# Optimization experiments

Measured on AMD Instinct MI355X. Metric: run time of the kernel, lower is better.

## Reference

```python
import jax, jax.numpy as jnp
import numpy as np

HEADS = 8
DIM_HEAD = 64

def setup_inputs() -> dict:
    key = jax.random.key(0)
    k1, k2, k3 = jax.random.split(key, 3)
    B, L, D = 8, 4096, 512
    hidden = HEADS * DIM_HEAD  # 512
    x = jax.random.normal(k1, (B, L, D), dtype=jnp.float32)
    # Conv1d(kernel_size=1) weights, squeezed to 2D matrices
    Wqkv = jax.random.normal(k2, (3 * hidden, D), dtype=jnp.float32) * (1.0 / np.sqrt(D))
    Wout = jax.random.normal(k3, (D, hidden), dtype=jnp.float32) * (1.0 / np.sqrt(hidden))
    bout = jnp.zeros((D,), dtype=jnp.float32)
    return {"x": x, "Wqkv": Wqkv, "Wout": Wout, "bout": bout}

def reference(x, Wqkv, Wout, bout):
    B, L, D = x.shape
    H, C = HEADS, DIM_HEAD
    # pointwise conv == linear over channel dim: (b, 3*H*C, l)
    qkv = jnp.einsum('bld,od->bol', x, Wqkv)
    qkv = qkv.reshape(B, 3, H, C, L)  # channel split order: (qkv, heads, c)
    q, k, v = qkv[:, 0], qkv[:, 1], qkv[:, 2]  # each (b, h, c, l)
    k = jax.nn.softmax(k, axis=-1)   # softmax over sequence
    q = jax.nn.softmax(q, axis=-2)   # softmax over feature dim (q_norm=True)
    context = jnp.einsum('bhdn,bhen->bhde', k, v)   # (b,h,c,c)
    out = jnp.einsum('bhde,bhdn->bhen', context, q)  # (b,h,c,l)
    out = out.reshape(B, H * C, L)
    y = jnp.einsum('bcl,dc->bld', out, Wout) + bout  # to_out + permute back
    return y
```

## Files before the change

### kernel.cpp

```cpp
#include <hip/hip_runtime.h>

#define L 4096
#define D 512
#define NCH 16

typedef __bf16 bf16x8 __attribute__((ext_vector_type(8)));
typedef float  f32x4  __attribute__((ext_vector_type(4)));

__device__ __forceinline__ void load_lds16(const void* g, void* l) {
    __builtin_amdgcn_global_load_lds(
        (const __attribute__((address_space(1))) void*)g,
        (__attribute__((address_space(3))) void*)l, 16, 0, 0);
}

__global__ __launch_bounds__(256) void f32_to_bf16(const float* __restrict__ in,
                                                   __bf16* __restrict__ out, int n8) {
    int i = blockIdx.x * 256 + threadIdx.x;
    if (i >= n8) return;
    const float4* p = (const float4*)in + (size_t)i * 2;
    float4 a = p[0], b = p[1];
    bf16x8 o = {(__bf16)a.x, (__bf16)a.y, (__bf16)a.z, (__bf16)a.w,
                (__bf16)b.x, (__bf16)b.y, (__bf16)b.z, (__bf16)b.w};
    *(bf16x8*)(out + (size_t)i * 8) = o;
}

template <int M, int N, int K, typename CT>
__global__ __launch_bounds__(256) void gemm_bf16_mfma(
    const __bf16* __restrict__ A, size_t aStride,
    const __bf16* __restrict__ B, size_t bStride,
    CT* __restrict__ C, size_t cStride,
    const float* __restrict__ bias) {
    __shared__ __align__(16) __bf16 sA[128 * 32];
    __shared__ __align__(16) __bf16 sB[128 * 32];
    const int b  = blockIdx.z;
    const int m0 = blockIdx.y * 128;
    const int n0 = blockIdx.x * 128;
    const int t    = threadIdx.x;
    const int wave = t >> 6, lane = t & 63;
    const int wm = (wave & 1) * 64, wn = (wave >> 1) * 64;
    const __bf16* Ab = A + (size_t)b * aStride;
    const __bf16* Bb = B + (size_t)b * bStride;
    CT* Cb = C + (size_t)b * cStride;

    f32x4 acc[4][4];
#pragma unroll
    for (int i = 0; i < 4; i++)
#pragma unroll
        for (int j = 0; j < 4; j++) acc[i][j] = (f32x4)(0.0f);

    const int fr = lane & 15;
    const int cq = lane >> 4;
    const int ko = (cq ^ ((fr >> 1) & 3)) * 8;

    for (int k0 = 0; k0 < K; k0 += 32) {
        __syncthreads();
#pragma unroll
        for (int c = 0; c < 2; c++) {
            const int idx = c * 256 + t;
            const int row = idx >> 2, cc = idx & 3;
            const int scc = cc ^ ((row >> 1) & 3);
            load_lds16(Ab + (size_t)(m0 + row) * K + k0 + scc * 8, &sA[idx * 8]);
            load_lds16(Bb + (size_t)(n0 + row) * K + k0 + scc * 8, &sB[idx * 8]);
        }
        __syncthreads();
        bf16x8 af[4], bfr[4];
#pragma unroll
        for (int i = 0; i < 4; i++) {
            af[i]  = *(const bf16x8*)&sA[(wm + i * 16 + fr) * 32 + ko];
            bfr[i] = *(const bf16x8*)&sB[(wn + i * 16 + fr) * 32 + ko];
        }
#pragma unroll
        for (int i = 0; i < 4; i++)
#pragma unroll
            for (int j = 0; j < 4; j++)
                acc[i][j] = __builtin_amdgcn_mfma_f32_16x16x32_bf16(af[i], bfr[j], acc[i][j], 0, 0, 0);
    }

    const int col = lane & 15, rbase = (lane >> 4) * 4;
#pragma unroll
    for (int j = 0; j < 4; j++) {
        const int n = n0 + wn + j * 16 + col;
        const float bv = bias ? bias[n] : 0.0f;
#pragma unroll
        for (int i = 0; i < 4; i++) {
#pragma unroll
            for (int r = 0; r < 4; r++) {
                const int m = m0 + wm + i * 16 + rbase + r;
                Cb[(size_t)m * N + n] = (CT)(acc[i][j][r] + bv);
            }
        }
    }
}

__global__ __launch_bounds__(256) void kstats(const __bf16* __restrict__ qkv,
                                              float2* __restrict__ stats) {
    const int r = blockIdx.x;
    const int b = r >> 9, hc = r & 511;
    const __bf16* row = qkv + (size_t)b * 1536 * L + (size_t)(512 + hc) * L;
    __shared__ float sred[4];
    const int t = threadIdx.x;
    const bf16x8* p = (const bf16x8*)row;
    bf16x8 c0 = p[t * 2], c1 = p[t * 2 + 1];
    float v[16];
    float m = -1e30f;
#pragma unroll
    for (int j = 0; j < 8; j++) {
        v[j] = (float)c0[j];
        v[8 + j] = (float)c1[j];
    }
#pragma unroll
    for (int j = 0; j < 16; j++) m = fmaxf(m, v[j]);
#pragma unroll
    for (int off = 32; off > 0; off >>= 1) m = fmaxf(m, __shfl_down(m, off, 64));
    if ((t & 63) == 0) sred[t >> 6] = m;
    __syncthreads();
    const float m4 = fmaxf(fmaxf(sred[0], sred[1]), fmaxf(sred[2], sred[3]));
    float s = 0.f;
#pragma unroll
    for (int j = 0; j < 16; j++) s += __expf(v[j] - m4);
#pragma unroll
    for (int off = 32; off > 0; off >>= 1) s += __shfl_down(s, off, 64);
    __syncthreads();
    if ((t & 63) == 0) sred[t >> 6] = s;
    __syncthreads();
    if (t == 0) {
        const float stot = sred[0] + sred[1] + sred[2] + sred[3];
        stats[r] = make_float2(m4, 1.0f / stot);
    }
}

__global__ __launch_bounds__(256) void context_partial(const __bf16* __restrict__ qkv,
                                                       const float2* __restrict__ stats,
                                                       float* __restrict__ ctx) {
    const int chunk = blockIdx.x;
    const int bh = blockIdx.y;
    const int b = bh >> 3, h = bh & 7;
    const __bf16* kbase = qkv + (size_t)b * 1536 * L + (size_t)(512 + h * 64) * L;
    const __bf16* vbase = qkv + (size_t)b * 1536 * L + (size_t)(1024 + h * 64) * L;
    __shared__ float sk[64][65];
    __shared__ float sv[64][65];
    __shared__ float smax[64];
    const int t = threadIdx.x;
    if (t < 64) smax[t] = stats[bh * 64 + t].x;
    const int tx = t % 16, ty = t / 16;
    float acc[4][4] = {};
    const int n_start = chunk * (L / NCH);
    __syncthreads();
    for (int ns = 0; ns < L / NCH; ns += 64) {
        const int n0 = n_start + ns;
        const int nn = t % 64, d0 = t / 64;
#pragma unroll
        for (int r = 0; r < 16; r++) {
            int d = d0 + r * 4;
            sk[d][nn] = __expf((float)kbase[(size_t)d * L + n0 + nn] - smax[d]);
            sv[d][nn] = (float)vbase[(size_t)d * L + n0 + nn];
        }
        __syncthreads();
#pragma unroll 8
        for (int q = 0; q < 64; q++) {
            float a[4], bb[4];
#pragma unroll
            for (int i = 0; i < 4; i++) a[i] = sk[ty * 4 + i][q];
#pragma unroll
            for (int j = 0; j < 4; j++) bb[j] = sv[tx * 4 + j][q];
#pragma unroll
            for (int i = 0; i < 4; i++)
#pragma unroll
                for (int j = 0; j < 4; j++) acc[i][j] += a[i] * bb[j];
        }
        __syncthreads();
    }
    float invs[4];
#pragma unroll
    for (int i = 0; i < 4; i++) invs[i] = stats[bh * 64 + ty * 4 + i].y;
    float* cp = ctx + ((size_t)chunk * 64 + bh) * 4096;
#pragma unroll
    for (int j = 0; j < 4; j++) {
        float4 v = make_float4(acc[0][j] * invs[0], acc[1][j] * invs[1],
                               acc[2][j] * invs[2], acc[3][j] * invs[3]);
        *(float4*)(cp + (tx * 4 + j) * 64 + ty * 4) = v;
    }
}

__global__ __launch_bounds__(256) void ctx_reduce(const float* __restrict__ ctx,
                                                  __bf16* __restrict__ ctxT) {
    const int bh = blockIdx.x >> 2, quarter = blockIdx.x & 3;
    const int t = threadIdx.x;
    const int idx = quarter * 1024 + t * 4;
    float4 s = make_float4(0.f, 0.f, 0.f, 0.f);
    for (int ch = 0; ch < NCH; ch++) {
        float4 p = *(const float4*)&ctx[((size_t)ch * 64 + bh) * 4096 + idx];
        s.x += p.x; s.y += p.y; s.z += p.z; s.w += p.w;
    }
    __bf16* o = ctxT + (size_t)bh * 4096 + idx;
    o[0] = (__bf16)s.x; o[1] = (__bf16)s.y; o[2] = (__bf16)s.z; o[3] = (__bf16)s.w;
}

#define SPS 66
__global__ __launch_bounds__(256) void pv_fused(__bf16* __restrict__ qkv,
                                                const __bf16* __restrict__ ctxT) {
    __shared__ __align__(16) __bf16 sp[256 * SPS];
    __shared__ __align__(16) __bf16 sctx[64 * SPS];
    __shared__ float sinv[256];
    const int tileN = blockIdx.x;
    const int bh = blockIdx.y;
    const int b = bh >> 3, h = bh & 7;
    const int t = threadIdx.x;
    const int n0 = tileN * 256;
    const __bf16* qbase = qkv + (size_t)b * 1536 * L + (size_t)(h * 64) * L;

    {
        const int e = t >> 2, c = t & 3;
        const bf16x8* src = (const bf16x8*)(ctxT + ((size_t)bh * 64 + e) * 64 + c * 16);
        *(bf16x8*)&sctx[e * SPS + c * 16] = src[0];
        *(bf16x8*)&sctx[e * SPS + c * 16 + 8] = src[1];
    }

    float m = -1e30f;
    float qv[64];
#pragma unroll
    for (int d = 0; d < 64; d++) {
        qv[d] = (float)qbase[(size_t)d * L + n0 + t];
        m = fmaxf(m, qv[d]);
    }
    float s = 0.f;
#pragma unroll
    for (int d0 = 0; d0 < 64; d0 += 8) {
        bf16x8 ek;
#pragma unroll
        for (int j = 0; j < 8; j++) {
            float e = __expf(qv[d0 + j] - m);
            s += e;
            ek[j] = (__bf16)e;
        }
        *(bf16x8*)&sp[t * SPS + d0] = ek;
    }
    sinv[t] = 1.0f / s;
    __syncthreads();

    const int wave = t >> 6, lane = t & 63;
    const int wm = wave * 64;
    const int fr = lane & 15, kq = (lane >> 4) * 8;
    f32x4 acc[4][4];
#pragma unroll
    for (int i = 0; i < 4; i++)
#pragma unroll
        for (int j = 0; j < 4; j++) acc[i][j] = (f32x4)(0.0f);
#pragma unroll
    for (int kh = 0; kh < 2; kh++) {
        bf16x8 af[4], bfr[4];
#pragma unroll
        for (int i = 0; i < 4; i++)
            af[i] = *(const bf16x8*)&sp[(wm + i * 16 + fr) * SPS + kh * 32 + kq];
#pragma unroll
        for (int j = 0; j < 4; j++)
            bfr[j] = *(const bf16x8*)&sctx[(j * 16 + fr) * SPS + kh * 32 + kq];
#pragma unroll
        for (int i = 0; i < 4; i++)
#pragma unroll
            for (int j = 0; j < 4; j++)
                acc[i][j] = __builtin_amdgcn_mfma_f32_16x16x32_bf16(af[i], bfr[j], acc[i][j], 0, 0, 0);
    }

    __bf16* ob = qkv + (size_t)b * 1536 * L + (size_t)512 * L;
    const int col = lane & 15, rbase = (lane >> 4) * 4;
#pragma unroll
    for (int i = 0; i < 4; i++) {
#pragma unroll
        for (int r = 0; r < 4; r++) {
            const int nl = wm + i * 16 + rbase + r;
            const float inv = sinv[nl];
            const size_t rowoff = (size_t)(n0 + nl) * 512 + h * 64;
#pragma unroll
            for (int j = 0; j < 4; j++)
                ob[rowoff + j * 16 + col] = (__bf16)(acc[i][j][r] * inv);
        }
    }
}

extern "C" void kernel_launch(void* const* d_in, const int* in_sizes, int n_in,
                              void* d_out, int out_size, void* d_ws, size_t ws_size,
                              hipStream_t stream) {
    const float* x    = (const float*)d_in[0];
    const float* Wqkv = (const float*)d_in[1];
    const float* Wout = (const float*)d_in[2];
    const float* bout = (const float*)d_in[3];
    float* y = (float*)d_out;

    __bf16* qkv   = (__bf16*)d_ws;
    float*  ctx   = (float*)(qkv + (size_t)8 * 1536 * L);
    __bf16* xb    = (__bf16*)(ctx + (size_t)NCH * 64 * 4096);
    __bf16* Wqb   = xb + (size_t)8 * 4096 * 512;
    __bf16* Wob   = Wqb + (size_t)1536 * 512;
    float2* stats = (float2*)(Wob + (size_t)512 * 512);
    __bf16* ctxT  = (__bf16*)(stats + 4096);

    f32_to_bf16<<<dim3((8 * 4096 * 512 / 8 + 255) / 256), 256, 0, stream>>>(x, xb, 8 * 4096 * 512 / 8);
    f32_to_bf16<<<dim3((1536 * 512 / 8 + 255) / 256), 256, 0, stream>>>(Wqkv, Wqb, 1536 * 512 / 8);
    f32_to_bf16<<<dim3((512 * 512 / 8 + 255) / 256), 256, 0, stream>>>(Wout, Wob, 512 * 512 / 8);

    gemm_bf16_mfma<1536, 4096, 512, __bf16><<<dim3(4096 / 128, 1536 / 128, 8), 256, 0, stream>>>(
        Wqb, 0, xb, (size_t)4096 * 512, qkv, (size_t)1536 * 4096, nullptr);

    kstats<<<dim3(4096), 256, 0, stream>>>(qkv, stats);
    context_partial<<<dim3(NCH, 64), 256, 0, stream>>>(qkv, stats, ctx);
    ctx_reduce<<<dim3(256), 256, 0, stream>>>(ctx, ctxT);
    pv_fused<<<dim3(L / 256, 64), 256, 0, stream>>>(qkv, ctxT);

    const __bf16* outT = qkv + (size_t)512 * L;
    gemm_bf16_mfma<4096, 512, 512, float><<<dim3(512 / 128, 4096 / 128, 8), 256, 0, stream>>>(
        outT, (size_t)1536 * L, Wob, 0, y, (size_t)4096 * 512, bout);
}
```

Measured before the change: 311.3 us.

## Use MFMA for context matmul, widen GEMM K-tile, merge conversion kernels

The scalar fp32 context kernel becomes a bf16 MFMA kernel. It stages exp(k - max) and v for a 256-position chunk in LDS, accumulates per wave, and reduces the four waves through LDS. The softmax 1/sum scaling and the transpose move into ctx_reduce. The shared GEMM now loads 64-wide K tiles with an 8-way XOR swizzle, halving the number of barrier-separated iterations. The three fp32-to-bf16 conversions are merged into one launch. Trade-offs: more LDS per block, and a precision loss from storing exp(k) as bf16.

```diff
diff --git a/kernel.cpp b/kernel.cpp
--- a/kernel.cpp
+++ b/kernel.cpp
@@ -13,15 +13,23 @@
         (__attribute__((address_space(3))) void*)l, 16, 0, 0);
 }
 
-__global__ __launch_bounds__(256) void f32_to_bf16(const float* __restrict__ in,
-                                                   __bf16* __restrict__ out, int n8) {
+#define NX8  (8 * 4096 * 512 / 8)
+#define NW18 (1536 * 512 / 8)
+#define NW28 (512 * 512 / 8)
+__global__ __launch_bounds__(256) void convert_all(const float* __restrict__ x,
+                                                   const float* __restrict__ Wq,
+                                                   const float* __restrict__ Wo,
+                                                   __bf16* __restrict__ dst) {
     int i = blockIdx.x * 256 + threadIdx.x;
-    if (i >= n8) return;
-    const float4* p = (const float4*)in + (size_t)i * 2;
-    float4 a = p[0], b = p[1];
+    if (i >= NX8 + NW18 + NW28) return;
+    const float* s;
+    if (i < NX8)             s = x  + (size_t)i * 8;
+    else if (i < NX8 + NW18) s = Wq + (size_t)(i - NX8) * 8;
+    else                     s = Wo + (size_t)(i - NX8 - NW18) * 8;
+    float4 a = ((const float4*)s)[0], b = ((const float4*)s)[1];
     bf16x8 o = {(__bf16)a.x, (__bf16)a.y, (__bf16)a.z, (__bf16)a.w,
                 (__bf16)b.x, (__bf16)b.y, (__bf16)b.z, (__bf16)b.w};
-    *(bf16x8*)(out + (size_t)i * 8) = o;
+    *(bf16x8*)(dst + (size_t)i * 8) = o;
 }
 
 template <int M, int N, int K, typename CT>
@@ -30,8 +38,8 @@
     const __bf16* __restrict__ B, size_t bStride,
     CT* __restrict__ C, size_t cStride,
     const float* __restrict__ bias) {
-    __shared__ __align__(16) __bf16 sA[128 * 32];
-    __shared__ __align__(16) __bf16 sB[128 * 32];
+    __shared__ __align__(16) __bf16 sA[128 * 64];
+    __shared__ __align__(16) __bf16 sB[128 * 64];
     const int b  = blockIdx.z;
     const int m0 = blockIdx.y * 128;
     const int n0 = blockIdx.x * 128;
@@ -49,34 +57,37 @@
         for (int j = 0; j < 4; j++) acc[i][j] = (f32x4)(0.0f);
 
     const int fr = lane & 15;
-    const int cq = lane >> 4;
-    const int ko = (cq ^ ((fr >> 1) & 3)) * 8;
-
-    for (int k0 = 0; k0 < K; k0 += 32) {
+    const int g  = lane >> 4;
+
+    for (int k0 = 0; k0 < K; k0 += 64) {
         __syncthreads();
 #pragma unroll
-        for (int c = 0; c < 2; c++) {
+        for (int c = 0; c < 4; c++) {
             const int idx = c * 256 + t;
-            const int row = idx >> 2, cc = idx & 3;
-            const int scc = cc ^ ((row >> 1) & 3);
+            const int row = idx >> 3, cc = idx & 7;
+            const int scc = cc ^ (row & 7);
             load_lds16(Ab + (size_t)(m0 + row) * K + k0 + scc * 8, &sA[idx * 8]);
             load_lds16(Bb + (size_t)(n0 + row) * K + k0 + scc * 8, &sB[idx * 8]);
         }
         __syncthreads();
-        bf16x8 af[4], bfr[4];
-#pragma unroll
-        for (int i = 0; i < 4; i++) {
-            af[i]  = *(const bf16x8*)&sA[(wm + i * 16 + fr) * 32 + ko];
-            bfr[i] = *(const bf16x8*)&sB[(wn + i * 16 + fr) * 32 + ko];
-        }
-#pragma unroll
-        for (int i = 0; i < 4; i++)
-#pragma unroll
-            for (int j = 0; j < 4; j++)
-                acc[i][j] = __builtin_amdgcn_mfma_f32_16x16x32_bf16(af[i], bfr[j], acc[i][j], 0, 0, 0);
-    }
-
-    const int col = lane & 15, rbase = (lane >> 4) * 4;
+#pragma unroll
+        for (int kh = 0; kh < 2; kh++) {
+            const int ko = ((kh * 4 + g) ^ (fr & 7)) * 8;
+            bf16x8 af[4], bfr[4];
+#pragma unroll
+            for (int i = 0; i < 4; i++) {
+                af[i]  = *(const bf16x8*)&sA[(wm + i * 16 + fr) * 64 + ko];
+                bfr[i] = *(const bf16x8*)&sB[(wn + i * 16 + fr) * 64 + ko];
+            }
+#pragma unroll
+            for (int i = 0; i < 4; i++)
+#pragma unroll
+                for (int j = 0; j < 4; j++)
+                    acc[i][j] = __builtin_amdgcn_mfma_f32_16x16x32_bf16(af[i], bfr[j], acc[i][j], 0, 0, 0);
+        }
+    }
+
+    const int col = lane & 15, rbase = g * 4;
 #pragma unroll
     for (int j = 0; j < 4; j++) {
         const int n = n0 + wn + j * 16 + col;
@@ -129,71 +140,105 @@
     }
 }
 
-__global__ __launch_bounds__(256) void context_partial(const __bf16* __restrict__ qkv,
-                                                       const float2* __restrict__ stats,
-                                                       float* __restrict__ ctx) {
+#define SKS 264
+__global__ __launch_bounds__(256) void context_mfma(const __bf16* __restrict__ qkv,
+                                                    const float2* __restrict__ stats,
+                                                    float* __restrict__ ctxp) {
+    __shared__ __align__(16) __bf16 smem[2 * 64 * SKS];
+    __shared__ float smax[64];
+    __bf16* sk = smem;
+    __bf16* sv = smem + 64 * SKS;
     const int chunk = blockIdx.x;
     const int bh = blockIdx.y;
     const int b = bh >> 3, h = bh & 7;
     const __bf16* kbase = qkv + (size_t)b * 1536 * L + (size_t)(512 + h * 64) * L;
     const __bf16* vbase = qkv + (size_t)b * 1536 * L + (size_t)(1024 + h * 64) * L;
-    __shared__ float sk[64][65];
-    __shared__ float sv[64][65];
-    __shared__ float smax[64];
     const int t = threadIdx.x;
     if (t < 64) smax[t] = stats[bh * 64 + t].x;
-    const int tx = t % 16, ty = t / 16;
-    float acc[4][4] = {};
-    const int n_start = chunk * (L / NCH);
-    __syncthreads();
-    for (int ns = 0; ns < L / NCH; ns += 64) {
-        const int n0 = n_start + ns;
-        const int nn = t % 64, d0 = t / 64;
-#pragma unroll
-        for (int r = 0; r < 16; r++) {
-            int d = d0 + r * 4;
-            sk[d][nn] = __expf((float)kbase[(size_t)d * L + n0 + nn] - smax[d]);
-            sv[d][nn] = (float)vbase[(size_t)d * L + n0 + nn];
-        }
-        __syncthreads();
-#pragma unroll 8
-        for (int q = 0; q < 64; q++) {
-            float a[4], bb[4];
-#pragma unroll
-            for (int i = 0; i < 4; i++) a[i] = sk[ty * 4 + i][q];
-#pragma unroll
-            for (int j = 0; j < 4; j++) bb[j] = sv[tx * 4 + j][q];
-#pragma unroll
-            for (int i = 0; i < 4; i++)
-#pragma unroll
-                for (int j = 0; j < 4; j++) acc[i][j] += a[i] * bb[j];
-        }
-        __syncthreads();
-    }
-    float invs[4];
-#pragma unroll
-    for (int i = 0; i < 4; i++) invs[i] = stats[bh * 64 + ty * 4 + i].y;
-    float* cp = ctx + ((size_t)chunk * 64 + bh) * 4096;
-#pragma unroll
-    for (int j = 0; j < 4; j++) {
-        float4 v = make_float4(acc[0][j] * invs[0], acc[1][j] * invs[1],
-                               acc[2][j] * invs[2], acc[3][j] * invs[3]);
-        *(float4*)(cp + (tx * 4 + j) * 64 + ty * 4) = v;
-    }
-}
-
-__global__ __launch_bounds__(256) void ctx_reduce(const float* __restrict__ ctx,
+    __syncthreads();
+
+    {
+        const int d = t >> 2, noff = (t & 3) * 64;
+        const int n0 = chunk * 256;
+        const __bf16* kp = kbase + (size_t)d * L + n0 + noff;
+        const __bf16* vp = vbase + (size_t)d * L + n0 + noff;
+        const float md = smax[d];
+#pragma unroll
+        for (int c = 0; c < 8; c++) {
+            bf16x8 kk = *(const bf16x8*)(kp + c * 8);
+            bf16x8 vv = *(const bf16x8*)(vp + c * 8);
+            bf16x8 ek;
+#pragma unroll
+            for (int j = 0; j < 8; j++) ek[j] = (__bf16)__expf((float)kk[j] - md);
+            *(bf16x8*)&sk[d * SKS + noff + c * 8] = ek;
+            *(bf16x8*)&sv[d * SKS + noff + c * 8] = vv;
+        }
+    }
+    __syncthreads();
+
+    const int wave = t >> 6, lane = t & 63;
+    const int fr = lane & 15, kq = (lane >> 4) * 8;
+    f32x4 acc[4][4];
+#pragma unroll
+    for (int i = 0; i < 4; i++)
+#pragma unroll
+        for (int j = 0; j < 4; j++) acc[i][j] = (f32x4)(0.0f);
+#pragma unroll
+    for (int kh = 0; kh < 2; kh++) {
+        const int koff = wave * 64 + kh * 32 + kq;
+        bf16x8 af[4], bfr[4];
+#pragma unroll
+        for (int i = 0; i < 4; i++) {
+            af[i]  = *(const bf16x8*)&sk[(i * 16 + fr) * SKS + koff];
+            bfr[i] = *(const bf16x8*)&sv[(i * 16 + fr) * SKS + koff];
+        }
+#pragma unroll
+        for (int i = 0; i < 4; i++)
+#pragma unroll
+            for (int j = 0; j < 4; j++)
+                acc[i][j] = __builtin_amdgcn_mfma_f32_16x16x32_bf16(af[i], bfr[j], acc[i][j], 0, 0, 0);
+    }
+    __syncthreads();
+
+    float* red = (float*)smem;
+    const int col = lane & 15, rbase = (lane >> 4) * 4;
+#pragma unroll
+    for (int i = 0; i < 4; i++)
+#pragma unroll
+        for (int j = 0; j < 4; j++)
+#pragma unroll
+            for (int r = 0; r < 4; r++) {
+                const int dd = i * 16 + rbase + r;
+                const int ee = j * 16 + col;
+                red[wave * 4096 + dd * 64 + ee] = acc[i][j][r];
+            }
+    __syncthreads();
+    float* cp = ctxp + ((size_t)chunk * 64 + bh) * 4096;
+#pragma unroll
+    for (int gg = 0; gg < 4; gg++) {
+        const int idx = t * 16 + gg * 4;
+        f32x4 s = *(const f32x4*)&red[idx];
+        s += *(const f32x4*)&red[4096 + idx];
+        s += *(const f32x4*)&red[8192 + idx];
+        s += *(const f32x4*)&red[12288 + idx];
+        *(f32x4*)&cp[idx] = s;
+    }
+}
+
+__global__ __launch_bounds__(256) void ctx_reduce(const float* __restrict__ ctxp,
+                                                  const float2* __restrict__ stats,
                                                   __bf16* __restrict__ ctxT) {
     const int bh = blockIdx.x >> 2, quarter = blockIdx.x & 3;
     const int t = threadIdx.x;
-    const int idx = quarter * 1024 + t * 4;
-    float4 s = make_float4(0.f, 0.f, 0.f, 0.f);
-    for (int ch = 0; ch < NCH; ch++) {
-        float4 p = *(const float4*)&ctx[((size_t)ch * 64 + bh) * 4096 + idx];
-        s.x += p.x; s.y += p.y; s.z += p.z; s.w += p.w;
-    }
-    __bf16* o = ctxT + (size_t)bh * 4096 + idx;
-    o[0] = (__bf16)s.x; o[1] = (__bf16)s.y; o[2] = (__bf16)s.z; o[3] = (__bf16)s.w;
+    const int flat = quarter * 1024 + t * 4;
+    const int d = flat >> 6, e0 = flat & 63;
+    f32x4 s = (f32x4)(0.0f);
+    for (int ch = 0; ch < NCH; ch++)
+        s += *(const f32x4*)&ctxp[((size_t)ch * 64 + bh) * 4096 + flat];
+    const float inv = stats[bh * 64 + d].y;
+    __bf16* o = ctxT + (size_t)bh * 4096;
+#pragma unroll
+    for (int j = 0; j < 4; j++) o[(e0 + j) * 64 + d] = (__bf16)(s[j] * inv);
 }
 
 #define SPS 66
@@ -288,23 +333,22 @@
     float* y = (float*)d_out;
 
     __bf16* qkv   = (__bf16*)d_ws;
-    float*  ctx   = (float*)(qkv + (size_t)8 * 1536 * L);
-    __bf16* xb    = (__bf16*)(ctx + (size_t)NCH * 64 * 4096);
+    float*  ctxp  = (float*)(qkv + (size_t)8 * 1536 * L);
+    __bf16* xb    = (__bf16*)(ctxp + (size_t)NCH * 64 * 4096);
     __bf16* Wqb   = xb + (size_t)8 * 4096 * 512;
     __bf16* Wob   = Wqb + (size_t)1536 * 512;
     float2* stats = (float2*)(Wob + (size_t)512 * 512);
     __bf16* ctxT  = (__bf16*)(stats + 4096);
 
-    f32_to_bf16<<<dim3((8 * 4096 * 512 / 8 + 255) / 256), 256, 0, stream>>>(x, xb, 8 * 4096 * 512 / 8);
-    f32_to_bf16<<<dim3((1536 * 512 / 8 + 255) / 256), 256, 0, stream>>>(Wqkv, Wqb, 1536 * 512 / 8);
-    f32_to_bf16<<<dim3((512 * 512 / 8 + 255) / 256), 256, 0, stream>>>(Wout, Wob, 512 * 512 / 8);
+    const int convBlocks = (NX8 + NW18 + NW28 + 255) / 256;
+    convert_all<<<dim3(convBlocks), 256, 0, stream>>>(x, Wqkv, Wout, xb);
 
     gemm_bf16_mfma<1536, 4096, 512, __bf16><<<dim3(4096 / 128, 1536 / 128, 8), 256, 0, stream>>>(
         Wqb, 0, xb, (size_t)4096 * 512, qkv, (size_t)1536 * 4096, nullptr);
 
     kstats<<<dim3(4096), 256, 0, stream>>>(qkv, stats);
-    context_partial<<<dim3(NCH, 64), 256, 0, stream>>>(qkv, stats, ctx);
-    ctx_reduce<<<dim3(256), 256, 0, stream>>>(ctx, ctxT);
+    context_mfma<<<dim3(NCH, 64), 256, 0, stream>>>(qkv, stats, ctxp);
+    ctx_reduce<<<dim3(256), 256, 0, stream>>>(ctxp, stats, ctxT);
     pv_fused<<<dim3(L / 256, 64), 256, 0, stream>>>(qkv, ctxT);
 
     const __bf16* outT = qkv + (size_t)512 * L;
```

New measurement: 284.8 us. -8.5%, faster.
